# Kernel optimization log

Measured on AMD Instinct MI355X. Metric: run time of the kernel, lower is better.

## Reference

```python
import jax, jax.numpy as jnp
import numpy as np

N_HEADS = 16
HEAD_DIM = 64  # d_model // n_heads
D_MODEL = 1024


def setup_inputs() -> dict:
    key = jax.random.key(0)
    ks = jax.random.split(key, 8)
    B, T = 4, 2048
    inp = {
        "query": jax.random.normal(ks[0], (B, T, D_MODEL), dtype=jnp.float32),
        "key": jax.random.normal(ks[1], (B, T, D_MODEL), dtype=jnp.float32),
        "value": jax.random.normal(ks[2], (B, T, D_MODEL), dtype=jnp.float32),
        "query_padding_masks": jnp.ones((B, T), dtype=jnp.int32),
        "key_padding_masks": jnp.ones((B, T), dtype=jnp.int32),
        # weights stored as [in, out]; Linear has bias=False
        "W_q": jax.random.normal(ks[3], (D_MODEL, D_MODEL), dtype=jnp.float32) / np.sqrt(D_MODEL),
        "W_k": jax.random.normal(ks[4], (D_MODEL, D_MODEL), dtype=jnp.float32) / np.sqrt(D_MODEL),
        "W_v": jax.random.normal(ks[5], (D_MODEL, D_MODEL), dtype=jnp.float32) / np.sqrt(D_MODEL),
        "W_o": jax.random.normal(ks[6], (D_MODEL, D_MODEL), dtype=jnp.float32) / np.sqrt(D_MODEL),
    }
    return inp


def reference(query, key, value, query_padding_masks, key_padding_masks, W_q, W_k, W_v, W_o):
    B, T_q, _ = query.shape
    T_k = key.shape[1]
    # projections -> [B, H, T, Dh]
    q = (query @ W_q).reshape(B, T_q, N_HEADS, HEAD_DIM).transpose(0, 2, 1, 3)
    k = (key @ W_k).reshape(B, T_k, N_HEADS, HEAD_DIM).transpose(0, 2, 1, 3)
    v = (value @ W_v).reshape(B, T_k, N_HEADS, HEAD_DIM).transpose(0, 2, 1, 3)
    scale = 1.0 / jnp.sqrt(jnp.float32(HEAD_DIM))
    scores = jnp.einsum("bhqd,bhkd->bhqk", q, k) * scale  # [B,H,Tq,Tk]
    # causal mask * key padding mask, shape [B,1,Tq,Tk]
    causal = jnp.tril(jnp.ones((T_q, T_k), dtype=bool))
    mask = causal[None, None, :, :] & (key_padding_masks[:, None, None, :] != 0)
    scores = jnp.where(mask, scores, -jnp.inf)
    attn = jax.nn.softmax(scores, axis=-1)
    # post-softmax query padding multiply (as in original)
    attn = attn * query_padding_masks[:, None, :, None].astype(attn.dtype)
    out = jnp.einsum("bhqk,bhkd->bhqd", attn, v)  # [B,H,Tq,Dh]
    out = out.transpose(0, 2, 1, 3).reshape(B, T_q, N_HEADS * HEAD_DIM)
    return out @ W_o
```

## Files before the change

kernel.cpp:

```cpp
#include <hip/hip_runtime.h>
#include <hip/hip_bf16.h>
#include <stdint.h>


typedef __attribute__((ext_vector_type(8))) short short8;
typedef __attribute__((ext_vector_type(4))) float f32x4;

__device__ __forceinline__ unsigned short f2bf(float f) {
  union { float f; unsigned u; } v; v.f = f;
  unsigned r = (v.u + 0x7fffu + ((v.u >> 16) & 1u)) >> 16;
  return (unsigned short)r;
}

__device__ __forceinline__ void gl_lds16(const void* g, void* l) {
  __builtin_amdgcn_global_load_lds((const __attribute__((address_space(1))) void*)g,
                                   (__attribute__((address_space(3))) void*)l, 16, 0, 0);
}

__global__ __launch_bounds__(256) void prep_w(const float* __restrict__ Wq,
                                              const float* __restrict__ Wk,
                                              const float* __restrict__ Wv,
                                              const float* __restrict__ Wo,
                                              unsigned short* __restrict__ WT) {
  int z = blockIdx.z;
  const float* W = (z == 0) ? Wq : (z == 1) ? Wk : (z == 2) ? Wv : Wo;
  unsigned short* dst = WT + (size_t)z * 1024 * 1024;
  int k0 = blockIdx.x * 64, n0 = blockIdx.y * 64;
  __shared__ float tile[64][65];
  int tid = threadIdx.x;
#pragma unroll
  for (int j = 0; j < 4; ++j) {
    int u = tid + j * 256;
    int row = u >> 4, c4 = u & 15;
    float4 v = *(const float4*)(W + (size_t)(k0 + row) * 1024 + n0 + c4 * 4);
    tile[row][c4 * 4 + 0] = v.x;
    tile[row][c4 * 4 + 1] = v.y;
    tile[row][c4 * 4 + 2] = v.z;
    tile[row][c4 * 4 + 3] = v.w;
  }
  __syncthreads();
#pragma unroll
  for (int j = 0; j < 2; ++j) {
    int u = tid + j * 256;
    int nrow = u >> 3, kc = u & 7;
    unsigned e[8];
#pragma unroll
    for (int i = 0; i < 8; ++i) e[i] = f2bf(tile[kc * 8 + i][nrow]);
    uint4 o;
    o.x = e[0] | (e[1] << 16); o.y = e[2] | (e[3] << 16);
    o.z = e[4] | (e[5] << 16); o.w = e[6] | (e[7] << 16);
    *(uint4*)(dst + (size_t)(n0 + nrow) * 1024 + k0 + kc * 8) = o;
  }
}

__global__ __launch_bounds__(256) void prep_x(const float* __restrict__ Xq,
                                              const float* __restrict__ Xk,
                                              const float* __restrict__ Xv,
                                              unsigned short* __restrict__ Xb) {
  int z = blockIdx.z;
  const float* src = (z == 0) ? Xq : (z == 1) ? Xk : Xv;
  unsigned short* dst = Xb + (size_t)z * 8388608;
  size_t i0 = ((size_t)blockIdx.x * 256 + threadIdx.x) * 8;
  float4 a = *(const float4*)(src + i0);
  float4 b = *(const float4*)(src + i0 + 4);
  uint4 o;
  o.x = f2bf(a.x) | ((unsigned)f2bf(a.y) << 16);
  o.y = f2bf(a.z) | ((unsigned)f2bf(a.w) << 16);
  o.z = f2bf(b.x) | ((unsigned)f2bf(b.y) << 16);
  o.w = f2bf(b.z) | ((unsigned)f2bf(b.w) << 16);
  *(uint4*)(dst + i0) = o;
}

__global__ __launch_bounds__(256) void proj_gemm(const unsigned short* __restrict__ Xb,
                                                 const unsigned short* __restrict__ WT,
                                                 unsigned short* __restrict__ Qb,
                                                 unsigned short* __restrict__ Kb,
                                                 unsigned short* __restrict__ VTb) {
  int z = blockIdx.z;
  const unsigned short* A = Xb + (size_t)z * 8388608;
  const unsigned short* Bt = WT + (size_t)z * 1024 * 1024;
  int m0 = blockIdx.x * 128, n0 = blockIdx.y * 128;
  __shared__ __align__(16) unsigned short As[128 * 32];
  __shared__ __align__(16) unsigned short Bs[128 * 32];
  int tid = threadIdx.x, w = tid >> 6, lane = tid & 63;
  int lr = lane & 15, lg = lane >> 4;
  int wm = w >> 1, wn = w & 1;
  f32x4 acc[4][4];
#pragma unroll
  for (int i = 0; i < 4; ++i)
#pragma unroll
    for (int j = 0; j < 4; ++j) acc[i][j] = (f32x4){0.f, 0.f, 0.f, 0.f};

  for (int k0 = 0; k0 < 1024; k0 += 32) {
#pragma unroll
    for (int c = 0; c < 2; ++c) {
      int base = c * 256 + w * 64;
      int u = base + lane;
      int row = u >> 2, sl = u & 3;
      int ssl = sl ^ (row & 3);
      gl_lds16(A + (size_t)(m0 + row) * 1024 + k0 + ssl * 8, &As[base * 8]);
      gl_lds16(Bt + (size_t)(n0 + row) * 1024 + k0 + ssl * 8, &Bs[base * 8]);
    }
    __syncthreads();
    short8 af[4], bfr[4];
#pragma unroll
    for (int mi = 0; mi < 4; ++mi) {
      int row = wm * 64 + mi * 16 + lr;
      af[mi] = *(const short8*)(&As[(row * 4 + (lg ^ (row & 3))) * 8]);
    }
#pragma unroll
    for (int ni = 0; ni < 4; ++ni) {
      int row = wn * 64 + ni * 16 + lr;
      bfr[ni] = *(const short8*)(&Bs[(row * 4 + (lg ^ (row & 3))) * 8]);
    }
#pragma unroll
    for (int mi = 0; mi < 4; ++mi)
#pragma unroll
      for (int ni = 0; ni < 4; ++ni)
        acc[mi][ni] = __builtin_amdgcn_mfma_f32_16x16x32_bf16(af[mi], bfr[ni], acc[mi][ni], 0, 0, 0);
    __syncthreads();
  }
#pragma unroll
  for (int mi = 0; mi < 4; ++mi)
#pragma unroll
    for (int ni = 0; ni < 4; ++ni)
#pragma unroll
      for (int r = 0; r < 4; ++r) {
        int m = m0 + wm * 64 + mi * 16 + lg * 4 + r;
        int n = n0 + wn * 64 + ni * 16 + lr;
        unsigned short cb = f2bf(acc[mi][ni][r]);
        int b = m >> 11, t = m & 2047;
        int h = n >> 6, d = n & 63;
        if (z == 0)
          Qb[((size_t)(b * 16 + h) * 2048 + t) * 64 + d] = cb;
        else if (z == 1)
          Kb[((size_t)(b * 16 + h) * 2048 + t) * 64 + d] = cb;
        else
          VTb[((size_t)(b * 16 + h) * 64 + d) * 2048 + t] = cb;
      }
}

__global__ __launch_bounds__(256) void attn_kernel(const unsigned short* __restrict__ Qb,
                                                   const unsigned short* __restrict__ Kb,
                                                   const unsigned short* __restrict__ VTb,
                                                   const int* __restrict__ qpm,
                                                   const int* __restrict__ kpm,
                                                   unsigned short* __restrict__ Ob) {
  int bh = blockIdx.x;
  int qi = (int)gridDim.y - 1 - (int)blockIdx.y;
  int b = bh >> 4, h = bh & 15;
  int q0 = qi * 64;
  int tid = threadIdx.x, w = tid >> 6, lane = tid & 63;
  int lr = lane & 15, lg = lane >> 4;
  __shared__ __align__(16) unsigned short Ks[64 * 72];
  __shared__ __align__(16) unsigned short Vs[64 * 72];
  __shared__ __align__(16) unsigned short Ps[4][16 * 72];

  int qrow = q0 + w * 16 + lr;
  const unsigned short* qp = Qb + ((size_t)bh * 2048 + qrow) * 64 + lg * 8;
  short8 qf0 = *(const short8*)qp;
  short8 qf1 = *(const short8*)(qp + 32);
  const unsigned short* Kbh = Kb + (size_t)bh * 2048 * 64;
  const unsigned short* Vbh = VTb + (size_t)bh * 64 * 2048;

  f32x4 o[4];
#pragma unroll
  for (int dt = 0; dt < 4; ++dt) o[dt] = (f32x4){0.f, 0.f, 0.f, 0.f};
  float m_run = -1e30f, l_run = 0.f;
  const float CS = 0.125f * 1.44269504f;

  int kv_end = q0 + 64;
  for (int kv0 = 0; kv0 < kv_end; kv0 += 64) {
    __syncthreads();
#pragma unroll
    for (int j = 0; j < 2; ++j) {
      int u = tid + j * 256;
      int row = u >> 3, sl = u & 7;
      *(uint4*)(&Ks[row * 72 + sl * 8]) = *(const uint4*)(Kbh + (size_t)(kv0 + row) * 64 + sl * 8);
      *(uint4*)(&Vs[row * 72 + sl * 8]) = *(const uint4*)(Vbh + (size_t)row * 2048 + kv0 + sl * 8);
    }
    unsigned long long kmask = __ballot(kpm[b * 2048 + kv0 + lane] != 0);
    __syncthreads();

    float s[16];
#pragma unroll
    for (int t = 0; t < 4; ++t) {
      short8 kf0 = *(const short8*)(&Ks[(t * 16 + lr) * 72 + lg * 8]);
      short8 kf1 = *(const short8*)(&Ks[(t * 16 + lr) * 72 + 32 + lg * 8]);
      f32x4 sa = (f32x4){0.f, 0.f, 0.f, 0.f};
      sa = __builtin_amdgcn_mfma_f32_16x16x32_bf16(kf0, qf0, sa, 0, 0, 0);
      sa = __builtin_amdgcn_mfma_f32_16x16x32_bf16(kf1, qf1, sa, 0, 0, 0);
#pragma unroll
      for (int r = 0; r < 4; ++r) {
        int kvl = t * 16 + lg * 4 + r;
        int kvg = kv0 + kvl;
        bool ok = (kvg <= qrow) && ((kmask >> kvl) & 1ull);
        s[t * 4 + r] = ok ? sa[r] : -1e30f;
      }
    }
    float pm = s[0];
#pragma unroll
    for (int i = 1; i < 16; ++i) pm = fmaxf(pm, s[i]);
    pm = fmaxf(pm, __shfl_xor(pm, 16));
    pm = fmaxf(pm, __shfl_xor(pm, 32));
    float mnew = fmaxf(m_run, pm);
    float fs = exp2f((m_run - mnew) * CS);
    float p[16], ps = 0.f;
#pragma unroll
    for (int i = 0; i < 16; ++i) {
      p[i] = exp2f((s[i] - mnew) * CS);
      ps += p[i];
    }
    ps += __shfl_xor(ps, 16);
    ps += __shfl_xor(ps, 32);
    l_run = l_run * fs + ps;
    m_run = mnew;
    float f4[4];
#pragma unroll
    for (int r = 0; r < 4; ++r) f4[r] = __shfl(fs, lg * 4 + r);
#pragma unroll
    for (int dt = 0; dt < 4; ++dt)
#pragma unroll
      for (int r = 0; r < 4; ++r) o[dt][r] *= f4[r];
#pragma unroll
    for (int t = 0; t < 4; ++t) {
      unsigned lo = f2bf(p[t * 4 + 0]) | ((unsigned)f2bf(p[t * 4 + 1]) << 16);
      unsigned hi = f2bf(p[t * 4 + 2]) | ((unsigned)f2bf(p[t * 4 + 3]) << 16);
      *(uint2*)(&Ps[w][lr * 72 + t * 16 + lg * 4]) = make_uint2(lo, hi);
    }
#pragma unroll
    for (int st = 0; st < 2; ++st) {
      short8 pa = *(const short8*)(&Ps[w][lr * 72 + st * 32 + lg * 8]);
#pragma unroll
      for (int dt = 0; dt < 4; ++dt) {
        short8 vf = *(const short8*)(&Vs[(dt * 16 + lr) * 72 + st * 32 + lg * 8]);
        o[dt] = __builtin_amdgcn_mfma_f32_16x16x32_bf16(pa, vf, o[dt], 0, 0, 0);
      }
    }
  }
  float l4[4], qm4[4];
#pragma unroll
  for (int r = 0; r < 4; ++r) {
    l4[r] = __shfl(l_run, lg * 4 + r);
    int qg = q0 + w * 16 + lg * 4 + r;
    qm4[r] = (qpm[b * 2048 + qg] != 0) ? 1.f : 0.f;
  }
#pragma unroll
  for (int dt = 0; dt < 4; ++dt)
#pragma unroll
    for (int r = 0; r < 4; ++r) {
      int qg = q0 + w * 16 + lg * 4 + r;
      float val = o[dt][r] * qm4[r] / l4[r];
      Ob[(size_t)(b * 2048 + qg) * 1024 + h * 64 + dt * 16 + lr] = f2bf(val);
    }
}

__global__ __launch_bounds__(256) void out_gemm(const unsigned short* __restrict__ Ab,
                                                const unsigned short* __restrict__ WoT,
                                                float* __restrict__ C) {
  int m0 = blockIdx.x * 128, n0 = blockIdx.y * 128;
  __shared__ __align__(16) unsigned short As[128 * 32];
  __shared__ __align__(16) unsigned short Bs[128 * 32];
  int tid = threadIdx.x, w = tid >> 6, lane = tid & 63;
  int lr = lane & 15, lg = lane >> 4;
  int wm = w >> 1, wn = w & 1;
  f32x4 acc[4][4];
#pragma unroll
  for (int i = 0; i < 4; ++i)
#pragma unroll
    for (int j = 0; j < 4; ++j) acc[i][j] = (f32x4){0.f, 0.f, 0.f, 0.f};

  for (int k0 = 0; k0 < 1024; k0 += 32) {
#pragma unroll
    for (int c = 0; c < 2; ++c) {
      int base = c * 256 + w * 64;
      int u = base + lane;
      int row = u >> 2, sl = u & 3;
      int ssl = sl ^ (row & 3);
      gl_lds16(Ab + (size_t)(m0 + row) * 1024 + k0 + ssl * 8, &As[base * 8]);
      gl_lds16(WoT + (size_t)(n0 + row) * 1024 + k0 + ssl * 8, &Bs[base * 8]);
    }
    __syncthreads();
    short8 af[4], bfr[4];
#pragma unroll
    for (int mi = 0; mi < 4; ++mi) {
      int row = wm * 64 + mi * 16 + lr;
      af[mi] = *(const short8*)(&As[(row * 4 + (lg ^ (row & 3))) * 8]);
    }
#pragma unroll
    for (int ni = 0; ni < 4; ++ni) {
      int row = wn * 64 + ni * 16 + lr;
      bfr[ni] = *(const short8*)(&Bs[(row * 4 + (lg ^ (row & 3))) * 8]);
    }
#pragma unroll
    for (int mi = 0; mi < 4; ++mi)
#pragma unroll
      for (int ni = 0; ni < 4; ++ni)
        acc[mi][ni] = __builtin_amdgcn_mfma_f32_16x16x32_bf16(af[mi], bfr[ni], acc[mi][ni], 0, 0, 0);
    __syncthreads();
  }
#pragma unroll
  for (int mi = 0; mi < 4; ++mi)
#pragma unroll
    for (int ni = 0; ni < 4; ++ni)
#pragma unroll
      for (int r = 0; r < 4; ++r) {
        int m = m0 + wm * 64 + mi * 16 + lg * 4 + r;
        int n = n0 + wn * 64 + ni * 16 + lr;
        C[(size_t)m * 1024 + n] = acc[mi][ni][r];
      }
}

extern "C" void kernel_launch(void* const* d_in, const int* in_sizes, int n_in,
                              void* d_out, int out_size, void* d_ws, size_t ws_size,
                              hipStream_t stream) {
  const float* q = (const float*)d_in[0];
  const float* k = (const float*)d_in[1];
  const float* v = (const float*)d_in[2];
  const int* qpm = (const int*)d_in[3];
  const int* kpm = (const int*)d_in[4];
  const float* Wq = (const float*)d_in[5];
  const float* Wk = (const float*)d_in[6];
  const float* Wv = (const float*)d_in[7];
  const float* Wo = (const float*)d_in[8];
  float* out = (float*)d_out;

  char* ws = (char*)d_ws;
  unsigned short* WT  = (unsigned short*)(ws);
  unsigned short* Xb  = (unsigned short*)(ws + ((size_t)8 << 20));
  unsigned short* Ob  = (unsigned short*)(ws + ((size_t)8 << 20));
  unsigned short* Qb  = (unsigned short*)(ws + ((size_t)56 << 20));
  unsigned short* Kb  = (unsigned short*)(ws + ((size_t)72 << 20));
  unsigned short* VTb = (unsigned short*)(ws + ((size_t)88 << 20));

  prep_w<<<dim3(16, 16, 4), 256, 0, stream>>>(Wq, Wk, Wv, Wo, WT);
  prep_x<<<dim3(4096, 1, 3), 256, 0, stream>>>(q, k, v, Xb);
  proj_gemm<<<dim3(64, 8, 3), 256, 0, stream>>>(Xb, WT, Qb, Kb, VTb);
  attn_kernel<<<dim3(64, 32), 256, 0, stream>>>(Qb, Kb, VTb, qpm, kpm, Ob);
  out_gemm<<<dim3(64, 8), 256, 0, stream>>>(Ob, WT + (size_t)3 * 1024 * 1024, out);
}
```

Measured before the change: 378.8 us.

## Widen attention query tile to 128 rows with swizzled async LDS loads

```diff
diff --git a/kernel.cpp b/kernel.cpp
--- a/kernel.cpp
+++ b/kernel.cpp
@@ -11,6 +11,18 @@
   unsigned r = (v.u + 0x7fffu + ((v.u >> 16) & 1u)) >> 16;
   return (unsigned short)r;
 }
+
+__device__ __forceinline__ unsigned pk2(float a, float b) {
+  __hip_bfloat162 h = __float22bfloat162_rn(make_float2(a, b));
+  union { __hip_bfloat162 h; unsigned u; } cv; cv.h = h;
+  return cv.u;
+}
+
+#if __has_builtin(__builtin_amdgcn_exp2f)
+#define EXP2(x) __builtin_amdgcn_exp2f(x)
+#else
+#define EXP2(x) exp2f(x)
+#endif
 
 __device__ __forceinline__ void gl_lds16(const void* g, void* l) {
   __builtin_amdgcn_global_load_lds((const __attribute__((address_space(1))) void*)g,
@@ -147,112 +159,158 @@
                                                    const int* __restrict__ kpm,
                                                    unsigned short* __restrict__ Ob) {
   int bh = blockIdx.x;
-  int qi = (int)gridDim.y - 1 - (int)blockIdx.y;
+  int qi = 15 - (int)blockIdx.y;
   int b = bh >> 4, h = bh & 15;
-  int q0 = qi * 64;
+  int q0 = qi * 128;
   int tid = threadIdx.x, w = tid >> 6, lane = tid & 63;
   int lr = lane & 15, lg = lane >> 4;
-  __shared__ __align__(16) unsigned short Ks[64 * 72];
-  __shared__ __align__(16) unsigned short Vs[64 * 72];
-  __shared__ __align__(16) unsigned short Ps[4][16 * 72];
-
-  int qrow = q0 + w * 16 + lr;
-  const unsigned short* qp = Qb + ((size_t)bh * 2048 + qrow) * 64 + lg * 8;
-  short8 qf0 = *(const short8*)qp;
-  short8 qf1 = *(const short8*)(qp + 32);
+  __shared__ __align__(16) unsigned short Ks[64 * 64];
+  __shared__ __align__(16) unsigned short Vs[64 * 64];
+  __shared__ __align__(16) unsigned short Ps[4][32 * 72];
+
   const unsigned short* Kbh = Kb + (size_t)bh * 2048 * 64;
   const unsigned short* Vbh = VTb + (size_t)bh * 64 * 2048;
-
-  f32x4 o[4];
-#pragma unroll
-  for (int dt = 0; dt < 4; ++dt) o[dt] = (f32x4){0.f, 0.f, 0.f, 0.f};
-  float m_run = -1e30f, l_run = 0.f;
+  int qb0 = q0 + w * 32;
+
+  short8 qf[2][2];
+#pragma unroll
+  for (int s = 0; s < 2; ++s) {
+    const unsigned short* qp = Qb + ((size_t)bh * 2048 + qb0 + s * 16 + lr) * 64 + lg * 8;
+    qf[s][0] = *(const short8*)qp;
+    qf[s][1] = *(const short8*)(qp + 32);
+  }
+
+  f32x4 o[2][4];
+  float m[2] = {-1e30f, -1e30f}, l[2] = {0.f, 0.f};
+#pragma unroll
+  for (int s = 0; s < 2; ++s)
+#pragma unroll
+    for (int dt = 0; dt < 4; ++dt) o[s][dt] = (f32x4){0.f, 0.f, 0.f, 0.f};
+
   const float CS = 0.125f * 1.44269504f;
-
-  int kv_end = q0 + 64;
-  for (int kv0 = 0; kv0 < kv_end; kv0 += 64) {
+  int ntiles = 2 * qi + 2;
+  for (int it = 0; it < ntiles; ++it) {
+    int kv0 = it * 64;
     __syncthreads();
 #pragma unroll
     for (int j = 0; j < 2; ++j) {
-      int u = tid + j * 256;
-      int row = u >> 3, sl = u & 7;
-      *(uint4*)(&Ks[row * 72 + sl * 8]) = *(const uint4*)(Kbh + (size_t)(kv0 + row) * 64 + sl * 8);
-      *(uint4*)(&Vs[row * 72 + sl * 8]) = *(const uint4*)(Vbh + (size_t)row * 2048 + kv0 + sl * 8);
+      int base = j * 256 + w * 64;
+      int u = base + lane;
+      int row = u >> 3, c = u & 7, cs = c ^ (row & 7);
+      gl_lds16(Kbh + (size_t)(kv0 + row) * 64 + cs * 8, &Ks[base * 8]);
+      gl_lds16(Vbh + (size_t)row * 2048 + kv0 + cs * 8, &Vs[base * 8]);
     }
     unsigned long long kmask = __ballot(kpm[b * 2048 + kv0 + lane] != 0);
     __syncthreads();
-
-    float s[16];
+    bool allk = (kmask == ~0ull);
+
+    short8 kf[4][2];
 #pragma unroll
     for (int t = 0; t < 4; ++t) {
-      short8 kf0 = *(const short8*)(&Ks[(t * 16 + lr) * 72 + lg * 8]);
-      short8 kf1 = *(const short8*)(&Ks[(t * 16 + lr) * 72 + 32 + lg * 8]);
-      f32x4 sa = (f32x4){0.f, 0.f, 0.f, 0.f};
-      sa = __builtin_amdgcn_mfma_f32_16x16x32_bf16(kf0, qf0, sa, 0, 0, 0);
-      sa = __builtin_amdgcn_mfma_f32_16x16x32_bf16(kf1, qf1, sa, 0, 0, 0);
+      int krow = t * 16 + lr;
+#pragma unroll
+      for (int c = 0; c < 2; ++c) {
+        int slot = (c * 4 + lg) ^ (krow & 7);
+        kf[t][c] = *(const short8*)(&Ks[krow * 64 + slot * 8]);
+      }
+    }
+
+    bool act[2];
+#pragma unroll
+    for (int s = 0; s < 2; ++s) {
+      int qb = qb0 + s * 16;
+      act[s] = (kv0 <= qb + 15);
+      if (!act[s]) continue;
+      float sv[16];
+#pragma unroll
+      for (int t = 0; t < 4; ++t) {
+        f32x4 sa = (f32x4){0.f, 0.f, 0.f, 0.f};
+        sa = __builtin_amdgcn_mfma_f32_16x16x32_bf16(kf[t][0], qf[s][0], sa, 0, 0, 0);
+        sa = __builtin_amdgcn_mfma_f32_16x16x32_bf16(kf[t][1], qf[s][1], sa, 0, 0, 0);
+#pragma unroll
+        for (int r = 0; r < 4; ++r) sv[t * 4 + r] = sa[r];
+      }
+      if (!(allk && kv0 + 63 <= qb)) {
+        int qrow = qb + lr;
+#pragma unroll
+        for (int t = 0; t < 4; ++t)
+#pragma unroll
+          for (int r = 0; r < 4; ++r) {
+            int kvl = t * 16 + lg * 4 + r;
+            bool ok = (kv0 + kvl <= qrow) && ((kmask >> kvl) & 1ull);
+            sv[t * 4 + r] = ok ? sv[t * 4 + r] : -1e30f;
+          }
+      }
+      float x0 = fmaxf(fmaxf(sv[0], sv[1]), fmaxf(sv[2], sv[3]));
+      float x1 = fmaxf(fmaxf(sv[4], sv[5]), fmaxf(sv[6], sv[7]));
+      float x2 = fmaxf(fmaxf(sv[8], sv[9]), fmaxf(sv[10], sv[11]));
+      float x3 = fmaxf(fmaxf(sv[12], sv[13]), fmaxf(sv[14], sv[15]));
+      float pm = fmaxf(fmaxf(x0, x1), fmaxf(x2, x3));
+      pm = fmaxf(pm, __shfl_xor(pm, 16));
+      pm = fmaxf(pm, __shfl_xor(pm, 32));
+      if (!__all(pm <= m[s] + 44.0f)) {
+        float mnew = fmaxf(m[s], pm);
+        float fs = EXP2((m[s] - mnew) * CS);
+        m[s] = mnew;
+        float f4[4];
+#pragma unroll
+        for (int r = 0; r < 4; ++r) f4[r] = __shfl(fs, lg * 4 + r);
+#pragma unroll
+        for (int dt = 0; dt < 4; ++dt)
+#pragma unroll
+          for (int r = 0; r < 4; ++r) o[s][dt][r] *= f4[r];
+        l[s] *= fs;
+      }
+#pragma unroll
+      for (int i = 0; i < 16; ++i) sv[i] = EXP2((sv[i] - m[s]) * CS);
+      float y0 = (sv[0] + sv[1]) + (sv[2] + sv[3]);
+      float y1 = (sv[4] + sv[5]) + (sv[6] + sv[7]);
+      float y2 = (sv[8] + sv[9]) + (sv[10] + sv[11]);
+      float y3 = (sv[12] + sv[13]) + (sv[14] + sv[15]);
+      float ps_ = (y0 + y1) + (y2 + y3);
+      ps_ += __shfl_xor(ps_, 16);
+      ps_ += __shfl_xor(ps_, 32);
+      l[s] += ps_;
+#pragma unroll
+      for (int t = 0; t < 4; ++t) {
+        unsigned lo = pk2(sv[t * 4 + 0], sv[t * 4 + 1]);
+        unsigned hi = pk2(sv[t * 4 + 2], sv[t * 4 + 3]);
+        *(uint2*)(&Ps[w][(s * 16 + lr) * 72 + t * 16 + lg * 4]) = make_uint2(lo, hi);
+      }
+    }
+#pragma unroll
+    for (int st = 0; st < 2; ++st) {
+      short8 pa0{}, pa1{};
+      if (act[0]) pa0 = *(const short8*)(&Ps[w][(0 * 16 + lr) * 72 + st * 32 + lg * 8]);
+      if (act[1]) pa1 = *(const short8*)(&Ps[w][(1 * 16 + lr) * 72 + st * 32 + lg * 8]);
+#pragma unroll
+      for (int dt = 0; dt < 4; ++dt) {
+        int vrow = dt * 16 + lr;
+        int slot = (st * 4 + lg) ^ (vrow & 7);
+        short8 vf = *(const short8*)(&Vs[vrow * 64 + slot * 8]);
+        if (act[0]) o[0][dt] = __builtin_amdgcn_mfma_f32_16x16x32_bf16(pa0, vf, o[0][dt], 0, 0, 0);
+        if (act[1]) o[1][dt] = __builtin_amdgcn_mfma_f32_16x16x32_bf16(pa1, vf, o[1][dt], 0, 0, 0);
+      }
+    }
+  }
+#pragma unroll
+  for (int s = 0; s < 2; ++s) {
+    float l4[4], qm4[4];
+#pragma unroll
+    for (int r = 0; r < 4; ++r) {
+      l4[r] = __shfl(l[s], lg * 4 + r);
+      int qg = q0 + w * 32 + s * 16 + lg * 4 + r;
+      qm4[r] = (qpm[b * 2048 + qg] != 0) ? 1.f : 0.f;
+    }
+#pragma unroll
+    for (int dt = 0; dt < 4; ++dt)
 #pragma unroll
       for (int r = 0; r < 4; ++r) {
-        int kvl = t * 16 + lg * 4 + r;
-        int kvg = kv0 + kvl;
-        bool ok = (kvg <= qrow) && ((kmask >> kvl) & 1ull);
-        s[t * 4 + r] = ok ? sa[r] : -1e30f;
-      }
-    }
-    float pm = s[0];
-#pragma unroll
-    for (int i = 1; i < 16; ++i) pm = fmaxf(pm, s[i]);
-    pm = fmaxf(pm, __shfl_xor(pm, 16));
-    pm = fmaxf(pm, __shfl_xor(pm, 32));
-    float mnew = fmaxf(m_run, pm);
-    float fs = exp2f((m_run - mnew) * CS);
-    float p[16], ps = 0.f;
-#pragma unroll
-    for (int i = 0; i < 16; ++i) {
-      p[i] = exp2f((s[i] - mnew) * CS);
-      ps += p[i];
-    }
-    ps += __shfl_xor(ps, 16);
-    ps += __shfl_xor(ps, 32);
-    l_run = l_run * fs + ps;
-    m_run = mnew;
-    float f4[4];
-#pragma unroll
-    for (int r = 0; r < 4; ++r) f4[r] = __shfl(fs, lg * 4 + r);
-#pragma unroll
-    for (int dt = 0; dt < 4; ++dt)
-#pragma unroll
-      for (int r = 0; r < 4; ++r) o[dt][r] *= f4[r];
-#pragma unroll
-    for (int t = 0; t < 4; ++t) {
-      unsigned lo = f2bf(p[t * 4 + 0]) | ((unsigned)f2bf(p[t * 4 + 1]) << 16);
-      unsigned hi = f2bf(p[t * 4 + 2]) | ((unsigned)f2bf(p[t * 4 + 3]) << 16);
-      *(uint2*)(&Ps[w][lr * 72 + t * 16 + lg * 4]) = make_uint2(lo, hi);
-    }
-#pragma unroll
-    for (int st = 0; st < 2; ++st) {
-      short8 pa = *(const short8*)(&Ps[w][lr * 72 + st * 32 + lg * 8]);
-#pragma unroll
-      for (int dt = 0; dt < 4; ++dt) {
-        short8 vf = *(const short8*)(&Vs[(dt * 16 + lr) * 72 + st * 32 + lg * 8]);
-        o[dt] = __builtin_amdgcn_mfma_f32_16x16x32_bf16(pa, vf, o[dt], 0, 0, 0);
-      }
-    }
-  }
-  float l4[4], qm4[4];
-#pragma unroll
-  for (int r = 0; r < 4; ++r) {
-    l4[r] = __shfl(l_run, lg * 4 + r);
-    int qg = q0 + w * 16 + lg * 4 + r;
-    qm4[r] = (qpm[b * 2048 + qg] != 0) ? 1.f : 0.f;
-  }
-#pragma unroll
-  for (int dt = 0; dt < 4; ++dt)
-#pragma unroll
-    for (int r = 0; r < 4; ++r) {
-      int qg = q0 + w * 16 + lg * 4 + r;
-      float val = o[dt][r] * qm4[r] / l4[r];
-      Ob[(size_t)(b * 2048 + qg) * 1024 + h * 64 + dt * 16 + lr] = f2bf(val);
-    }
+        int qg = q0 + w * 32 + s * 16 + lg * 4 + r;
+        float val = o[s][dt][r] * qm4[r] / l4[r];
+        Ob[(size_t)(b * 2048 + qg) * 1024 + h * 64 + dt * 16 + lr] = f2bf(val);
+      }
+  }
 }
 
 __global__ __launch_bounds__(256) void out_gemm(const unsigned short* __restrict__ Ab,
@@ -336,6 +394,6 @@
   prep_w<<<dim3(16, 16, 4), 256, 0, stream>>>(Wq, Wk, Wv, Wo, WT);
   prep_x<<<dim3(4096, 1, 3), 256, 0, stream>>>(q, k, v, Xb);
   proj_gemm<<<dim3(64, 8, 3), 256, 0, stream>>>(Xb, WT, Qb, Kb, VTb);
-  attn_kernel<<<dim3(64, 32), 256, 0, stream>>>(Qb, Kb, VTb, qpm, kpm, Ob);
+  attn_kernel<<<dim3(64, 16), 256, 0, stream>>>(Qb, Kb, VTb, qpm, kpm, Ob);
   out_gemm<<<dim3(64, 8), 256, 0, stream>>>(Ob, WT + (size_t)3 * 1024 * 1024, out);
 }
```

Measured after the change: 363.4 us. -4.1%, faster.
